# Kernel optimization log

Measured on AMD Instinct MI355X. Metric: run time of the kernel, lower is better.

Reference implementation:

```python
import jax, jax.numpy as jnp
import numpy as np

N_NODES = 10000
N_EDGES = 320000
HIDDEN = 256
HEADS = 8
HEAD_DIM = HIDDEN // HEADS  # 32
NEG_SLOPE = 0.2


def setup_inputs() -> dict:
    key = jax.random.key(0)
    ks = jax.random.split(key, 12)
    x = jax.random.normal(ks[0], (N_NODES, HIDDEN), dtype=jnp.float32)
    edges_idx = jax.random.randint(ks[1], (2, N_EDGES), 0, N_NODES, dtype=jnp.int64)
    s = 1.0 / np.sqrt(HIDDEN)
    # layer 1 params
    W1 = jax.random.normal(ks[2], (HIDDEN, HEADS * HEAD_DIM), dtype=jnp.float32) * s
    a_src1 = jax.random.normal(ks[3], (HEADS, HEAD_DIM), dtype=jnp.float32) * s
    a_dst1 = jax.random.normal(ks[4], (HEADS, HEAD_DIM), dtype=jnp.float32) * s
    b1 = jnp.zeros((HEADS * HEAD_DIM,), dtype=jnp.float32)
    # layer 2 params
    W2 = jax.random.normal(ks[5], (HIDDEN, HEADS * HEAD_DIM), dtype=jnp.float32) * s
    a_src2 = jax.random.normal(ks[6], (HEADS, HEAD_DIM), dtype=jnp.float32) * s
    a_dst2 = jax.random.normal(ks[7], (HEADS, HEAD_DIM), dtype=jnp.float32) * s
    b2 = jnp.zeros((HEADS * HEAD_DIM,), dtype=jnp.float32)
    return {"x": x, "edges_idx": edges_idx,
            "W1": W1, "a_src1": a_src1, "a_dst1": a_dst1, "b1": b1,
            "W2": W2, "a_src2": a_src2, "a_dst2": a_dst2, "b2": b2}


def gat_conv(x, src, dst, W, a_src, a_dst, b):
    """PyG GATConv (concat=True, negative_slope=0.2), dropout in eval mode."""
    N = x.shape[0]
    h = (x @ W).reshape(N, HEADS, HEAD_DIM)          # [N,H,C]
    alpha_s = jnp.einsum('nhc,hc->nh', h, a_src)     # [N,H]
    alpha_d = jnp.einsum('nhc,hc->nh', h, a_dst)     # [N,H]
    e = alpha_s[src] + alpha_d[dst]                  # [E,H]
    e = jnp.where(e > 0, e, NEG_SLOPE * e)           # leaky_relu
    # scatter-softmax over incoming edges of each dst node
    m = jax.ops.segment_max(e, dst, num_segments=N)  # [N,H]
    ex = jnp.exp(e - m[dst])                         # [E,H]
    denom = jax.ops.segment_sum(ex, dst, num_segments=N)  # [N,H]
    alpha = ex / (denom[dst] + 1e-16)                # [E,H]
    msg = h[src] * alpha[:, :, None]                 # [E,H,C]
    out = jax.ops.segment_sum(msg, dst, num_segments=N)   # [N,H,C]
    return out.reshape(N, HEADS * HEAD_DIM) + b


def reference(x, edges_idx, W1, a_src1, a_dst1, b1, W2, a_src2, a_dst2, b2):
    src = edges_idx[0]
    dst = edges_idx[1]
    h = gat_conv(x, src, dst, W1, a_src1, a_dst1, b1)
    h = jax.nn.elu(h)
    out = gat_conv(h, src, dst, W2, a_src2, a_dst2, b2)
    return out
```

## Files before the change

kernel.cpp:

```cpp
#include <hip/hip_runtime.h>
#include <hip/hip_bf16.h>
#include <hip/hip_fp16.h>

#define N_NODES 10000
#define N_EDGES 320000
#define HIDDEN 256
#define HEADS 8
#define HEAD_DIM 32
#define NEG_SLOPE 0.2f
#define CAP 80

typedef __attribute__((ext_vector_type(8))) short short8;
typedef __attribute__((ext_vector_type(8))) _Float16 half8;
typedef __attribute__((ext_vector_type(4))) float f32x4;

__device__ __forceinline__ void bf16_split(float v, unsigned short& hi, unsigned short& lo) {
    __hip_bfloat16 hb = __float2bfloat16(v);
    float hf = __bfloat162float(hb);
    __hip_bfloat16 lb = __float2bfloat16(v - hf);
    hi = *reinterpret_cast<unsigned short*>(&hb);
    lo = *reinterpret_cast<unsigned short*>(&lb);
}

__global__ __launch_bounds__(256) void prep_kernel(
    const float* __restrict__ W1, const float* __restrict__ W2,
    const int* __restrict__ src, const int* __restrict__ dst,
    unsigned short* __restrict__ w1h, unsigned short* __restrict__ w1l,
    unsigned short* __restrict__ w2h, unsigned short* __restrict__ w2l,
    int* __restrict__ counts, int* __restrict__ csr_src) {
    int b = blockIdx.x;
    int tid = threadIdx.x;
    if (b < 512) {
        int i = b * 256 + tid;
        int which = i >> 16;
        int rem = i & 0xFFFF;
        int k = rem >> 8, n = rem & 255;
        const float* W = which ? W2 : W1;
        unsigned short* wh = which ? w2h : w1h;
        unsigned short* wl = which ? w2l : w1l;
        unsigned short h, l;
        bf16_split(W[k * 256 + n], h, l);
        wh[n * 256 + k] = h;
        wl[n * 256 + k] = l;
    } else {
        int e = (b - 512) * 256 + tid;
        int d = dst[e];
        int rank = atomicAdd(&counts[d], 1);
        csr_src[d * CAP + rank] = src[e];
    }
}

template <int AFP32>
__global__ __launch_bounds__(256) void gemm_mfma_kernel(
    const float* __restrict__ Axf,
    const unsigned short* __restrict__ Ah, const unsigned short* __restrict__ Al,
    const unsigned short* __restrict__ BhT, const unsigned short* __restrict__ BlT,
    _Float16* __restrict__ hH, const float* __restrict__ a_src,
    const float* __restrict__ a_dst, float* __restrict__ alpha_s,
    float* __restrict__ alpha_d) {
    __shared__ __align__(16) unsigned short sAh[80 * 40];
    __shared__ __align__(16) unsigned short sAl[80 * 40];
    __shared__ __align__(16) unsigned short sBh[128 * 40];
    __shared__ __align__(16) unsigned short sBl[128 * 40];
    __shared__ __align__(16) _Float16 sOut[80 * 264];
    const int tid = threadIdx.x;
    const int w = tid >> 6, lane = tid & 63;
    const int col = lane & 15, quad = lane >> 4;
    const int m0 = blockIdx.y * 80, n0 = blockIdx.x * 128;

    f32x4 acc[5][2] = {};

    float4 raf[2][3];
    uint4 rau[2][3];
    uint4 rb[2][4];

#define LOAD_A(k0, SS)                                                          \
    if (AFP32) {                                                                \
        _Pragma("unroll") for (int i = 0; i < 3; ++i) {                         \
            int t = tid + i * 256;                                              \
            if (t < 640) {                                                      \
                int row = t >> 3, seg = t & 7;                                  \
                raf[SS][i] = *(const float4*)&Axf[(size_t)(m0 + row) * 256 + (k0) + seg * 4]; \
            }                                                                   \
        }                                                                       \
    } else {                                                                    \
        _Pragma("unroll") for (int i = 0; i < 3; ++i) {                         \
            int t = tid + i * 256;                                              \
            if (t < 640) {                                                      \
                int tt = t < 320 ? t : t - 320;                                 \
                int row = tt >> 2, seg = tt & 3;                                \
                const unsigned short* P = t < 320 ? Ah : Al;                    \
                rau[SS][i] = *(const uint4*)&P[(size_t)(m0 + row) * 256 + (k0) + seg * 8]; \
            }                                                                   \
        }                                                                       \
    }
#define LOAD_B(k0, SS)                                                          \
    _Pragma("unroll") for (int i = 0; i < 4; ++i) {                             \
        int t = tid + i * 256;                                                  \
        int tt = t < 512 ? t : t - 512;                                         \
        int row = tt >> 2, seg = tt & 3;                                        \
        const unsigned short* P = t < 512 ? BhT : BlT;                          \
        rb[SS][i] = *(const uint4*)&P[(size_t)(n0 + row) * 256 + (k0) + seg * 8]; \
    }
#define WRITE_A(SS)                                                             \
    if (AFP32) {                                                                \
        _Pragma("unroll") for (int i = 0; i < 3; ++i) {                         \
            int t = tid + i * 256;                                              \
            if (t < 640) {                                                      \
                int row = t >> 3, seg = t & 7;                                  \
                float4 v = raf[SS][i];                                          \
                ushort4 hh, ll;                                                 \
                unsigned short hb, lb;                                          \
                bf16_split(v.x, hb, lb); hh.x = hb; ll.x = lb;                  \
                bf16_split(v.y, hb, lb); hh.y = hb; ll.y = lb;                  \
                bf16_split(v.z, hb, lb); hh.z = hb; ll.z = lb;                  \
                bf16_split(v.w, hb, lb); hh.w = hb; ll.w = lb;                  \
                *(ushort4*)&sAh[row * 40 + seg * 4] = hh;                       \
                *(ushort4*)&sAl[row * 40 + seg * 4] = ll;                       \
            }                                                                   \
        }                                                                       \
    } else {                                                                    \
        _Pragma("unroll") for (int i = 0; i < 3; ++i) {                         \
            int t = tid + i * 256;                                              \
            if (t < 640) {                                                      \
                int tt = t < 320 ? t : t - 320;                                 \
                int row = tt >> 2, seg = tt & 3;                                \
                unsigned short* Sp = t < 320 ? sAh : sAl;                       \
                *(uint4*)&Sp[row * 40 + seg * 8] = rau[SS][i];                  \
            }                                                                   \
        }                                                                       \
    }
#define WRITE_B(SS)                                                             \
    _Pragma("unroll") for (int i = 0; i < 4; ++i) {                             \
        int t = tid + i * 256;                                                  \
        int tt = t < 512 ? t : t - 512;                                         \
        int row = tt >> 2, seg = tt & 3;                                        \
        unsigned short* Sp = t < 512 ? sBh : sBl;                               \
        *(uint4*)&Sp[row * 40 + seg * 8] = rb[SS][i];                           \
    }

    LOAD_A(0, 0)
    LOAD_B(0, 0)
    LOAD_A(32, 1)
    LOAD_B(32, 1)

#pragma unroll
    for (int ks = 0; ks < 8; ++ks) {
        WRITE_A(ks & 1)
        WRITE_B(ks & 1)
        __syncthreads();

        if (ks < 6) {
            LOAD_A((ks + 2) * 32, ks & 1)
            LOAD_B((ks + 2) * 32, ks & 1)
        }

        short8 bh0 = *(const short8*)&sBh[(w * 32 + col) * 40 + quad * 8];
        short8 bl0 = *(const short8*)&sBl[(w * 32 + col) * 40 + quad * 8];
        short8 bh1 = *(const short8*)&sBh[(w * 32 + 16 + col) * 40 + quad * 8];
        short8 bl1 = *(const short8*)&sBl[(w * 32 + 16 + col) * 40 + quad * 8];
#pragma unroll
        for (int rt = 0; rt < 5; ++rt) {
            short8 ah = *(const short8*)&sAh[(rt * 16 + col) * 40 + quad * 8];
            short8 al = *(const short8*)&sAl[(rt * 16 + col) * 40 + quad * 8];
            acc[rt][0] = __builtin_amdgcn_mfma_f32_16x16x32_bf16(ah, bh0, acc[rt][0], 0, 0, 0);
            acc[rt][0] = __builtin_amdgcn_mfma_f32_16x16x32_bf16(ah, bl0, acc[rt][0], 0, 0, 0);
            acc[rt][0] = __builtin_amdgcn_mfma_f32_16x16x32_bf16(al, bh0, acc[rt][0], 0, 0, 0);
            acc[rt][1] = __builtin_amdgcn_mfma_f32_16x16x32_bf16(ah, bh1, acc[rt][1], 0, 0, 0);
            acc[rt][1] = __builtin_amdgcn_mfma_f32_16x16x32_bf16(ah, bl1, acc[rt][1], 0, 0, 0);
            acc[rt][1] = __builtin_amdgcn_mfma_f32_16x16x32_bf16(al, bh1, acc[rt][1], 0, 0, 0);
        }
        __syncthreads();
    }
#undef LOAD_A
#undef LOAD_B
#undef WRITE_A
#undef WRITE_B

    const int head = blockIdx.x * 4 + w;
    float as0 = a_src[n0 + w * 32 + col];
    float as1 = a_src[n0 + w * 32 + 16 + col];
    float ad0 = a_dst[n0 + w * 32 + col];
    float ad1 = a_dst[n0 + w * 32 + 16 + col];
#pragma unroll
    for (int rt = 0; rt < 5; ++rt) {
#pragma unroll
        for (int r = 0; r < 4; ++r) {
            int row = rt * 16 + quad * 4 + r;
            sOut[row * 264 + w * 32 + col]      = (_Float16)acc[rt][0][r];
            sOut[row * 264 + w * 32 + 16 + col] = (_Float16)acc[rt][1][r];
            float ps = acc[rt][0][r] * as0 + acc[rt][1][r] * as1;
            float pd = acc[rt][0][r] * ad0 + acc[rt][1][r] * ad1;
#pragma unroll
            for (int m = 1; m < 16; m <<= 1) {
                ps += __shfl_xor(ps, m);
                pd += __shfl_xor(pd, m);
            }
            if (col == 0) {
                int gm = m0 + row;
                alpha_s[gm * HEADS + head] = ps;
                alpha_d[gm * HEADS + head] = pd;
            }
        }
    }
    __syncthreads();
#pragma unroll
    for (int i = 0; i < 5; ++i) {
        int t = tid + i * 256;
        int row = t >> 4, seg = t & 15;
        *(half8*)&hH[(size_t)(m0 + row) * 256 + n0 + seg * 8] =
            *(const half8*)&sOut[row * 264 + seg * 8];
    }
}

__global__ __launch_bounds__(256) void aggregate_kernel(
    const int* __restrict__ counts, const int* __restrict__ csr_src,
    const float* __restrict__ alpha_s, const float* __restrict__ alpha_d,
    const _Float16* __restrict__ hH, const float* __restrict__ bias,
    float* __restrict__ outf, unsigned short* __restrict__ oh,
    unsigned short* __restrict__ ol, int mode) {
    const int tid = threadIdx.x;
    const int w = tid >> 6, lane = tid & 63;
    const int ph = blockIdx.x / 2500;
    const int d = (blockIdx.x - ph * 2500) * 4 + w;
    const int q = lane >> 4, fl = lane & 15;
    const int hd = ph * 4 + (fl >> 2);
    const float ad = alpha_d[d * HEADS + hd];
    const int n = counts[d];
    const int* __restrict__ bucket = csr_src + d * CAP;
    const int qb = q * 4;

    const _Float16* hp = hH + ph * 128 + fl * 8;
    float acc[8] = {};
    float den = 0.f;

    int4 s0_ = make_int4(0, 0, 0, 0), s1_ = s0_, s2_ = s0_, s3_ = s0_, s4_ = s0_;
    if (n > 0)  s0_ = *(const int4*)&bucket[qb];
    if (n > 16) s1_ = *(const int4*)&bucket[qb + 16];
    if (n > 32) s2_ = *(const int4*)&bucket[qb + 32];
    if (n > 48) s3_ = *(const int4*)&bucket[qb + 48];
    if (n > 64) s4_ = *(const int4*)&bucket[qb + 64];

#define AGG_DECL(t) float al##t##0, al##t##1, al##t##2, al##t##3;               \
                    half8 hv##t##0, hv##t##1, hv##t##2, hv##t##3;
    AGG_DECL(0) AGG_DECL(1) AGG_DECL(2) AGG_DECL(3) AGG_DECL(4)

#define AGG_CLAMP(x) ((x) < 0 ? 0 : ((x) > 9999 ? 9999 : (x)))
#define AGG_GATHER(t, sv)                                                       \
    {                                                                           \
        int i0_ = AGG_CLAMP((sv).x), i1_ = AGG_CLAMP((sv).y);                   \
        int i2_ = AGG_CLAMP((sv).z), i3_ = AGG_CLAMP((sv).w);                   \
        al##t##0 = alpha_s[i0_ * HEADS + hd];                                   \
        al##t##1 = alpha_s[i1_ * HEADS + hd];                                   \
        al##t##2 = alpha_s[i2_ * HEADS + hd];                                   \
        al##t##3 = alpha_s[i3_ * HEADS + hd];                                   \
        hv##t##0 = *(const half8*)&hp[(size_t)i0_ * HIDDEN];                    \
        hv##t##1 = *(const half8*)&hp[(size_t)i1_ * HIDDEN];                    \
        hv##t##2 = *(const half8*)&hp[(size_t)i2_ * HIDDEN];                    \
        hv##t##3 = *(const half8*)&hp[(size_t)i3_ * HIDDEN];                    \
    }
#define AGG_COMPUTE(t, base)                                                    \
    {                                                                           \
        int b0_ = (base) + qb;                                                  \
        float e0 = al##t##0 + ad; e0 = e0 > 0.f ? e0 : NEG_SLOPE * e0;          \
        float e1 = al##t##1 + ad; e1 = e1 > 0.f ? e1 : NEG_SLOPE * e1;          \
        float e2 = al##t##2 + ad; e2 = e2 > 0.f ? e2 : NEG_SLOPE * e2;          \
        float e3 = al##t##3 + ad; e3 = e3 > 0.f ? e3 : NEG_SLOPE * e3;          \
        if (b0_ >= n)     e0 = -1e30f;                                          \
        if (b0_ + 1 >= n) e1 = -1e30f;                                          \
        if (b0_ + 2 >= n) e2 = -1e30f;                                          \
        if (b0_ + 3 >= n) e3 = -1e30f;                                          \
        float ev0 = __expf(e0), ev1 = __expf(e1);                               \
        float ev2 = __expf(e2), ev3 = __expf(e3);                               \
        den += (ev0 + ev1) + (ev2 + ev3);                                       \
        _Pragma("unroll") for (int j = 0; j < 8; ++j)                           \
            acc[j] += (float)hv##t##0[j] * ev0 + (float)hv##t##1[j] * ev1 +     \
                      (float)hv##t##2[j] * ev2 + (float)hv##t##3[j] * ev3;      \
    }

    if (n > 0)  AGG_GATHER(0, s0_)
    if (n > 16) AGG_GATHER(1, s1_)
    if (n > 0)  AGG_COMPUTE(0, 0)
    if (n > 32) AGG_GATHER(2, s2_)
    if (n > 16) AGG_COMPUTE(1, 16)
    if (n > 48) AGG_GATHER(3, s3_)
    if (n > 32) AGG_COMPUTE(2, 32)
    if (n > 64) AGG_GATHER(4, s4_)
    if (n > 48) AGG_COMPUTE(3, 48)
    if (n > 64) AGG_COMPUTE(4, 64)

#undef AGG_DECL
#undef AGG_CLAMP
#undef AGG_GATHER
#undef AGG_COMPUTE

#pragma unroll
    for (int j = 0; j < 8; ++j) acc[j] += __shfl_xor(acc[j], 16);
    den += __shfl_xor(den, 16);
#pragma unroll
    for (int j = 0; j < 8; ++j) acc[j] += __shfl_xor(acc[j], 32);
    den += __shfl_xor(den, 32);

    if (q == 0) {
        float inv = 1.f / (den + 1e-16f);
        float v[8];
#pragma unroll
        for (int j = 0; j < 8; ++j)
            v[j] = acc[j] * inv + bias[ph * 128 + fl * 8 + j];
        size_t oidx = (size_t)d * HIDDEN + ph * 128 + fl * 8;
        if (mode == 1) {
            unsigned short hb[8], lb[8];
#pragma unroll
            for (int j = 0; j < 8; ++j) {
                v[j] = v[j] > 0.f ? v[j] : (__expf(v[j]) - 1.f);
                bf16_split(v[j], hb[j], lb[j]);
            }
            *(ushort4*)&oh[oidx]     = make_ushort4(hb[0], hb[1], hb[2], hb[3]);
            *(ushort4*)&oh[oidx + 4] = make_ushort4(hb[4], hb[5], hb[6], hb[7]);
            *(ushort4*)&ol[oidx]     = make_ushort4(lb[0], lb[1], lb[2], lb[3]);
            *(ushort4*)&ol[oidx + 4] = make_ushort4(lb[4], lb[5], lb[6], lb[7]);
        } else {
            *(float4*)&outf[oidx]     = make_float4(v[0], v[1], v[2], v[3]);
            *(float4*)&outf[oidx + 4] = make_float4(v[4], v[5], v[6], v[7]);
        }
    }
}

extern "C" void kernel_launch(void* const* d_in, const int* in_sizes, int n_in,
                              void* d_out, int out_size, void* d_ws, size_t ws_size,
                              hipStream_t stream) {
    const float* x      = (const float*)d_in[0];
    const int*   edges  = (const int*)d_in[1];
    const float* W1     = (const float*)d_in[2];
    const float* as1    = (const float*)d_in[3];
    const float* ad1    = (const float*)d_in[4];
    const float* b1     = (const float*)d_in[5];
    const float* W2     = (const float*)d_in[6];
    const float* as2    = (const float*)d_in[7];
    const float* ad2    = (const float*)d_in[8];
    const float* b2     = (const float*)d_in[9];
    float* out = (float*)d_out;

    const int* src = edges;
    const int* dst = edges + N_EDGES;

    const size_t NF = (size_t)N_NODES * HIDDEN;
    const size_t NH = (size_t)N_NODES * HEADS;

    char* base = (char*)d_ws;
    _Float16* hH = (_Float16*)base;             base += NF * 2;
    unsigned short* x2h = (unsigned short*)base; base += NF * 2;
    unsigned short* x2l = (unsigned short*)base; base += NF * 2;
    float* alpha_s = (float*)base;              base += NH * 4;
    float* alpha_d = (float*)base;              base += NH * 4;
    unsigned short* w1h = (unsigned short*)base; base += 65536 * 2;
    unsigned short* w1l = (unsigned short*)base; base += 65536 * 2;
    unsigned short* w2h = (unsigned short*)base; base += 65536 * 2;
    unsigned short* w2l = (unsigned short*)base; base += 65536 * 2;
    int* csr_src = (int*)base;                  base += (size_t)N_NODES * CAP * 4;
    int* counts  = (int*)base;                  base += (size_t)N_NODES * 4;

    dim3 gemm_grid(2, 125);
    const int EB = (N_EDGES + 255) / 256;
    const int AGG_B = 2500 * 2;

    hipMemsetAsync(counts, 0, N_NODES * sizeof(int), stream);
    prep_kernel<<<512 + EB, 256, 0, stream>>>(W1, W2, src, dst,
                                              w1h, w1l, w2h, w2l, counts, csr_src);

    gemm_mfma_kernel<1><<<gemm_grid, 256, 0, stream>>>(
        x, nullptr, nullptr, w1h, w1l, hH, as1, ad1, alpha_s, alpha_d);
    aggregate_kernel<<<AGG_B, 256, 0, stream>>>(counts, csr_src, alpha_s, alpha_d,
                                                hH, b1, nullptr, x2h, x2l, 1);

    gemm_mfma_kernel<0><<<gemm_grid, 256, 0, stream>>>(
        nullptr, x2h, x2l, w2h, w2l, hH, as2, ad2, alpha_s, alpha_d);
    aggregate_kernel<<<AGG_B, 256, 0, stream>>>(counts, csr_src, alpha_s, alpha_d,
                                                hH, b2, out, nullptr, nullptr, 0);
}
```

Baseline: 198.3 us.

## Fuse prep, GEMM and aggregation into two persistent kernels with grid barriers

Replaces the memset-plus-five-launch sequence with two persistent kernels of 250 blocks × 512 threads. Inside them, software grid barriers (atomic counter plus spin) separate the prep, GEMM and aggregation phases. The intent is to remove kernel launch gaps and tail effects between stages. Only 4 of 8 waves do MFMA work in the GEMM phase, and aggregation runs as a grid-stride loop over fewer resident waves. That lowers the latency hiding available for the gather-heavy aggregation. The barrier also relies on all 250 blocks being co-resident.

```diff
diff --git a/kernel.cpp b/kernel.cpp
--- a/kernel.cpp
+++ b/kernel.cpp
@@ -9,6 +9,8 @@
 #define HEAD_DIM 32
 #define NEG_SLOPE 0.2f
 #define CAP 80
+#define NBLK 250
+#define TPB 512
 
 typedef __attribute__((ext_vector_type(8))) short short8;
 typedef __attribute__((ext_vector_type(8))) _Float16 half8;
@@ -22,16 +24,27 @@
     lo = *reinterpret_cast<unsigned short*>(&lb);
 }
 
-__global__ __launch_bounds__(256) void prep_kernel(
+__device__ __forceinline__ void grid_barrier(int* ctr) {
+    __syncthreads();
+    if (threadIdx.x == 0) {
+        __threadfence();
+        atomicAdd(ctr, 1);
+        while (__hip_atomic_load(ctr, __ATOMIC_RELAXED, __HIP_MEMORY_SCOPE_AGENT) < NBLK) {
+            __builtin_amdgcn_s_sleep(2);
+        }
+        __threadfence();
+    }
+    __syncthreads();
+}
+
+__device__ __forceinline__ void prep_phase(
+    int b, int tid,
     const float* __restrict__ W1, const float* __restrict__ W2,
     const int* __restrict__ src, const int* __restrict__ dst,
     unsigned short* __restrict__ w1h, unsigned short* __restrict__ w1l,
     unsigned short* __restrict__ w2h, unsigned short* __restrict__ w2l,
     int* __restrict__ counts, int* __restrict__ csr_src) {
-    int b = blockIdx.x;
-    int tid = threadIdx.x;
-    if (b < 512) {
-        int i = b * 256 + tid;
+    for (int i = b * TPB + tid; i < 131072; i += NBLK * TPB) {
         int which = i >> 16;
         int rem = i & 0xFFFF;
         int k = rem >> 8, n = rem & 255;
@@ -42,8 +55,8 @@
         bf16_split(W[k * 256 + n], h, l);
         wh[n * 256 + k] = h;
         wl[n * 256 + k] = l;
-    } else {
-        int e = (b - 512) * 256 + tid;
+    }
+    for (int e = b * TPB + tid; e < N_EDGES; e += NBLK * TPB) {
         int d = dst[e];
         int rank = atomicAdd(&counts[d], 1);
         csr_src[d * CAP + rank] = src[e];
@@ -51,7 +64,8 @@
 }
 
 template <int AFP32>
-__global__ __launch_bounds__(256) void gemm_mfma_kernel(
+__device__ __forceinline__ void gemm_phase(
+    int b, int tid,
     const float* __restrict__ Axf,
     const unsigned short* __restrict__ Ah, const unsigned short* __restrict__ Al,
     const unsigned short* __restrict__ BhT, const unsigned short* __restrict__ BlT,
@@ -63,29 +77,28 @@
     __shared__ __align__(16) unsigned short sBh[128 * 40];
     __shared__ __align__(16) unsigned short sBl[128 * 40];
     __shared__ __align__(16) _Float16 sOut[80 * 264];
-    const int tid = threadIdx.x;
+
     const int w = tid >> 6, lane = tid & 63;
     const int col = lane & 15, quad = lane >> 4;
-    const int m0 = blockIdx.y * 80, n0 = blockIdx.x * 128;
+    const int m0 = (b >> 1) * 80, n0 = (b & 1) * 128;
 
     f32x4 acc[5][2] = {};
-
-    float4 raf[2][3];
-    uint4 rau[2][3];
-    uint4 rb[2][4];
+    float4 raf[2][2];
+    uint4 rau[2][2];
+    uint4 rb[2][2];
 
 #define LOAD_A(k0, SS)                                                          \
     if (AFP32) {                                                                \
-        _Pragma("unroll") for (int i = 0; i < 3; ++i) {                         \
-            int t = tid + i * 256;                                              \
+        _Pragma("unroll") for (int i = 0; i < 2; ++i) {                         \
+            int t = tid + i * 512;                                              \
             if (t < 640) {                                                      \
                 int row = t >> 3, seg = t & 7;                                  \
                 raf[SS][i] = *(const float4*)&Axf[(size_t)(m0 + row) * 256 + (k0) + seg * 4]; \
             }                                                                   \
         }                                                                       \
     } else {                                                                    \
-        _Pragma("unroll") for (int i = 0; i < 3; ++i) {                         \
-            int t = tid + i * 256;                                              \
+        _Pragma("unroll") for (int i = 0; i < 2; ++i) {                         \
+            int t = tid + i * 512;                                              \
             if (t < 640) {                                                      \
                 int tt = t < 320 ? t : t - 320;                                 \
                 int row = tt >> 2, seg = tt & 3;                                \
@@ -95,8 +108,8 @@
         }                                                                       \
     }
 #define LOAD_B(k0, SS)                                                          \
-    _Pragma("unroll") for (int i = 0; i < 4; ++i) {                             \
-        int t = tid + i * 256;                                                  \
+    _Pragma("unroll") for (int i = 0; i < 2; ++i) {                             \
+        int t = tid + i * 512;                                                  \
         int tt = t < 512 ? t : t - 512;                                         \
         int row = tt >> 2, seg = tt & 3;                                        \
         const unsigned short* P = t < 512 ? BhT : BlT;                          \
@@ -104,8 +117,8 @@
     }
 #define WRITE_A(SS)                                                             \
     if (AFP32) {                                                                \
-        _Pragma("unroll") for (int i = 0; i < 3; ++i) {                         \
-            int t = tid + i * 256;                                              \
+        _Pragma("unroll") for (int i = 0; i < 2; ++i) {                         \
+            int t = tid + i * 512;                                              \
             if (t < 640) {                                                      \
                 int row = t >> 3, seg = t & 7;                                  \
                 float4 v = raf[SS][i];                                          \
@@ -120,8 +133,8 @@
             }                                                                   \
         }                                                                       \
     } else {                                                                    \
-        _Pragma("unroll") for (int i = 0; i < 3; ++i) {                         \
-            int t = tid + i * 256;                                              \
+        _Pragma("unroll") for (int i = 0; i < 2; ++i) {                         \
+            int t = tid + i * 512;                                              \
             if (t < 640) {                                                      \
                 int tt = t < 320 ? t : t - 320;                                 \
                 int row = tt >> 2, seg = tt & 3;                                \
@@ -131,8 +144,8 @@
         }                                                                       \
     }
 #define WRITE_B(SS)                                                             \
-    _Pragma("unroll") for (int i = 0; i < 4; ++i) {                             \
-        int t = tid + i * 256;                                                  \
+    _Pragma("unroll") for (int i = 0; i < 2; ++i) {                             \
+        int t = tid + i * 512;                                                  \
         int tt = t < 512 ? t : t - 512;                                         \
         int row = tt >> 2, seg = tt & 3;                                        \
         unsigned short* Sp = t < 512 ? sBh : sBl;                               \
@@ -155,20 +168,22 @@
             LOAD_B((ks + 2) * 32, ks & 1)
         }
 
-        short8 bh0 = *(const short8*)&sBh[(w * 32 + col) * 40 + quad * 8];
-        short8 bl0 = *(const short8*)&sBl[(w * 32 + col) * 40 + quad * 8];
-        short8 bh1 = *(const short8*)&sBh[(w * 32 + 16 + col) * 40 + quad * 8];
-        short8 bl1 = *(const short8*)&sBl[(w * 32 + 16 + col) * 40 + quad * 8];
-#pragma unroll
-        for (int rt = 0; rt < 5; ++rt) {
-            short8 ah = *(const short8*)&sAh[(rt * 16 + col) * 40 + quad * 8];
-            short8 al = *(const short8*)&sAl[(rt * 16 + col) * 40 + quad * 8];
-            acc[rt][0] = __builtin_amdgcn_mfma_f32_16x16x32_bf16(ah, bh0, acc[rt][0], 0, 0, 0);
-            acc[rt][0] = __builtin_amdgcn_mfma_f32_16x16x32_bf16(ah, bl0, acc[rt][0], 0, 0, 0);
-            acc[rt][0] = __builtin_amdgcn_mfma_f32_16x16x32_bf16(al, bh0, acc[rt][0], 0, 0, 0);
-            acc[rt][1] = __builtin_amdgcn_mfma_f32_16x16x32_bf16(ah, bh1, acc[rt][1], 0, 0, 0);
-            acc[rt][1] = __builtin_amdgcn_mfma_f32_16x16x32_bf16(ah, bl1, acc[rt][1], 0, 0, 0);
-            acc[rt][1] = __builtin_amdgcn_mfma_f32_16x16x32_bf16(al, bh1, acc[rt][1], 0, 0, 0);
+        if (w < 4) {
+            short8 bh0 = *(const short8*)&sBh[(w * 32 + col) * 40 + quad * 8];
+            short8 bl0 = *(const short8*)&sBl[(w * 32 + col) * 40 + quad * 8];
+            short8 bh1 = *(const short8*)&sBh[(w * 32 + 16 + col) * 40 + quad * 8];
+            short8 bl1 = *(const short8*)&sBl[(w * 32 + 16 + col) * 40 + quad * 8];
+#pragma unroll
+            for (int rt = 0; rt < 5; ++rt) {
+                short8 ah = *(const short8*)&sAh[(rt * 16 + col) * 40 + quad * 8];
+                short8 al = *(const short8*)&sAl[(rt * 16 + col) * 40 + quad * 8];
+                acc[rt][0] = __builtin_amdgcn_mfma_f32_16x16x32_bf16(ah, bh0, acc[rt][0], 0, 0, 0);
+                acc[rt][0] = __builtin_amdgcn_mfma_f32_16x16x32_bf16(ah, bl0, acc[rt][0], 0, 0, 0);
+                acc[rt][0] = __builtin_amdgcn_mfma_f32_16x16x32_bf16(al, bh0, acc[rt][0], 0, 0, 0);
+                acc[rt][1] = __builtin_amdgcn_mfma_f32_16x16x32_bf16(ah, bh1, acc[rt][1], 0, 0, 0);
+                acc[rt][1] = __builtin_amdgcn_mfma_f32_16x16x32_bf16(ah, bl1, acc[rt][1], 0, 0, 0);
+                acc[rt][1] = __builtin_amdgcn_mfma_f32_16x16x32_bf16(al, bh1, acc[rt][1], 0, 0, 0);
+            }
         }
         __syncthreads();
     }
@@ -177,95 +192,77 @@
 #undef WRITE_A
 #undef WRITE_B
 
-    const int head = blockIdx.x * 4 + w;
-    float as0 = a_src[n0 + w * 32 + col];
-    float as1 = a_src[n0 + w * 32 + 16 + col];
-    float ad0 = a_dst[n0 + w * 32 + col];
-    float ad1 = a_dst[n0 + w * 32 + 16 + col];
-#pragma unroll
-    for (int rt = 0; rt < 5; ++rt) {
-#pragma unroll
-        for (int r = 0; r < 4; ++r) {
-            int row = rt * 16 + quad * 4 + r;
-            sOut[row * 264 + w * 32 + col]      = (_Float16)acc[rt][0][r];
-            sOut[row * 264 + w * 32 + 16 + col] = (_Float16)acc[rt][1][r];
-            float ps = acc[rt][0][r] * as0 + acc[rt][1][r] * as1;
-            float pd = acc[rt][0][r] * ad0 + acc[rt][1][r] * ad1;
-#pragma unroll
-            for (int m = 1; m < 16; m <<= 1) {
-                ps += __shfl_xor(ps, m);
-                pd += __shfl_xor(pd, m);
+    if (w < 4) {
+        const int head = (b & 1) * 4 + w;
+        float as0 = a_src[n0 + w * 32 + col];
+        float as1 = a_src[n0 + w * 32 + 16 + col];
+        float ad0 = a_dst[n0 + w * 32 + col];
+        float ad1 = a_dst[n0 + w * 32 + 16 + col];
+#pragma unroll
+        for (int rt = 0; rt < 5; ++rt) {
+#pragma unroll
+            for (int r = 0; r < 4; ++r) {
+                int row = rt * 16 + quad * 4 + r;
+                sOut[row * 264 + w * 32 + col]      = (_Float16)acc[rt][0][r];
+                sOut[row * 264 + w * 32 + 16 + col] = (_Float16)acc[rt][1][r];
+                float ps = acc[rt][0][r] * as0 + acc[rt][1][r] * as1;
+                float pd = acc[rt][0][r] * ad0 + acc[rt][1][r] * ad1;
+#pragma unroll
+                for (int m = 1; m < 16; m <<= 1) {
+                    ps += __shfl_xor(ps, m);
+                    pd += __shfl_xor(pd, m);
+                }
+                if (col == 0) {
+                    int gm = m0 + row;
+                    alpha_s[gm * HEADS + head] = ps;
+                    alpha_d[gm * HEADS + head] = pd;
+                }
             }
-            if (col == 0) {
-                int gm = m0 + row;
-                alpha_s[gm * HEADS + head] = ps;
-                alpha_d[gm * HEADS + head] = pd;
-            }
         }
     }
     __syncthreads();
 #pragma unroll
-    for (int i = 0; i < 5; ++i) {
-        int t = tid + i * 256;
-        int row = t >> 4, seg = t & 15;
-        *(half8*)&hH[(size_t)(m0 + row) * 256 + n0 + seg * 8] =
-            *(const half8*)&sOut[row * 264 + seg * 8];
-    }
-}
-
-__global__ __launch_bounds__(256) void aggregate_kernel(
+    for (int i = 0; i < 3; ++i) {
+        int t = tid + i * 512;
+        if (t < 1280) {
+            int row = t >> 4, seg = t & 15;
+            *(half8*)&hH[(size_t)(m0 + row) * 256 + n0 + seg * 8] =
+                *(const half8*)&sOut[row * 264 + seg * 8];
+        }
+    }
+}
+
+template <int MODE>
+__device__ __forceinline__ void agg_phase(
+    int b, int tid,
     const int* __restrict__ counts, const int* __restrict__ csr_src,
     const float* __restrict__ alpha_s, const float* __restrict__ alpha_d,
     const _Float16* __restrict__ hH, const float* __restrict__ bias,
     float* __restrict__ outf, unsigned short* __restrict__ oh,
-    unsigned short* __restrict__ ol, int mode) {
-    const int tid = threadIdx.x;
+    unsigned short* __restrict__ ol) {
     const int w = tid >> 6, lane = tid & 63;
-    const int ph = blockIdx.x / 2500;
-    const int d = (blockIdx.x - ph * 2500) * 4 + w;
     const int q = lane >> 4, fl = lane & 15;
-    const int hd = ph * 4 + (fl >> 2);
-    const float ad = alpha_d[d * HEADS + hd];
-    const int n = counts[d];
-    const int* __restrict__ bucket = csr_src + d * CAP;
     const int qb = q * 4;
-
-    const _Float16* hp = hH + ph * 128 + fl * 8;
-    float acc[8] = {};
-    float den = 0.f;
-
-    int4 s0_ = make_int4(0, 0, 0, 0), s1_ = s0_, s2_ = s0_, s3_ = s0_, s4_ = s0_;
-    if (n > 0)  s0_ = *(const int4*)&bucket[qb];
-    if (n > 16) s1_ = *(const int4*)&bucket[qb + 16];
-    if (n > 32) s2_ = *(const int4*)&bucket[qb + 32];
-    if (n > 48) s3_ = *(const int4*)&bucket[qb + 48];
-    if (n > 64) s4_ = *(const int4*)&bucket[qb + 64];
-
-#define AGG_DECL(t) float al##t##0, al##t##1, al##t##2, al##t##3;               \
-                    half8 hv##t##0, hv##t##1, hv##t##2, hv##t##3;
-    AGG_DECL(0) AGG_DECL(1) AGG_DECL(2) AGG_DECL(3) AGG_DECL(4)
+    const int wg = b * 8 + w;
 
 #define AGG_CLAMP(x) ((x) < 0 ? 0 : ((x) > 9999 ? 9999 : (x)))
-#define AGG_GATHER(t, sv)                                                       \
+#define AGG_ROUND(sv, base)                                                     \
     {                                                                           \
         int i0_ = AGG_CLAMP((sv).x), i1_ = AGG_CLAMP((sv).y);                   \
         int i2_ = AGG_CLAMP((sv).z), i3_ = AGG_CLAMP((sv).w);                   \
-        al##t##0 = alpha_s[i0_ * HEADS + hd];                                   \
-        al##t##1 = alpha_s[i1_ * HEADS + hd];                                   \
-        al##t##2 = alpha_s[i2_ * HEADS + hd];                                   \
-        al##t##3 = alpha_s[i3_ * HEADS + hd];                                   \
-        hv##t##0 = *(const half8*)&hp[(size_t)i0_ * HIDDEN];                    \
-        hv##t##1 = *(const half8*)&hp[(size_t)i1_ * HIDDEN];                    \
-        hv##t##2 = *(const half8*)&hp[(size_t)i2_ * HIDDEN];                    \
-        hv##t##3 = *(const half8*)&hp[(size_t)i3_ * HIDDEN];                    \
-    }
-#define AGG_COMPUTE(t, base)                                                    \
-    {                                                                           \
+        float al0 = alpha_s[i0_ * HEADS + hd];                                  \
+        float al1 = alpha_s[i1_ * HEADS + hd];                                  \
+        float al2 = alpha_s[i2_ * HEADS + hd];                                  \
+        float al3 = alpha_s[i3_ * HEADS + hd];                                  \
+        half8 h0 = *(const half8*)&hp[(size_t)i0_ * HIDDEN];                    \
+        half8 h1 = *(const half8*)&hp[(size_t)i1_ * HIDDEN];                    \
+        half8 h2 = *(const half8*)&hp[(size_t)i2_ * HIDDEN];                    \
+        half8 h3 = *(const half8*)&hp[(size_t)i3_ * HIDDEN];                    \
         int b0_ = (base) + qb;                                                  \
-        float e0 = al##t##0 + ad; e0 = e0 > 0.f ? e0 : NEG_SLOPE * e0;          \
-        float e1 = al##t##1 + ad; e1 = e1 > 0.f ? e1 : NEG_SLOPE * e1;          \
-        float e2 = al##t##2 + ad; e2 = e2 > 0.f ? e2 : NEG_SLOPE * e2;          \
-        float e3 = al##t##3 + ad; e3 = e3 > 0.f ? e3 : NEG_SLOPE * e3;          \
+        float e0 = al0 + ad; e0 = e0 > 0.f ? e0 : NEG_SLOPE * e0;               \
+        float e1 = al1 + ad; e1 = e1 > 0.f ? e1 : NEG_SLOPE * e1;               \
+        float e2 = al2 + ad; e2 = e2 > 0.f ? e2 : NEG_SLOPE * e2;               \
+        float e3 = al3 + ad; e3 = e3 > 0.f ? e3 : NEG_SLOPE * e3;               \
         if (b0_ >= n)     e0 = -1e30f;                                          \
         if (b0_ + 1 >= n) e1 = -1e30f;                                          \
         if (b0_ + 2 >= n) e2 = -1e30f;                                          \
@@ -274,56 +271,98 @@
         float ev2 = __expf(e2), ev3 = __expf(e3);                               \
         den += (ev0 + ev1) + (ev2 + ev3);                                       \
         _Pragma("unroll") for (int j = 0; j < 8; ++j)                           \
-            acc[j] += (float)hv##t##0[j] * ev0 + (float)hv##t##1[j] * ev1 +     \
-                      (float)hv##t##2[j] * ev2 + (float)hv##t##3[j] * ev3;      \
-    }
-
-    if (n > 0)  AGG_GATHER(0, s0_)
-    if (n > 16) AGG_GATHER(1, s1_)
-    if (n > 0)  AGG_COMPUTE(0, 0)
-    if (n > 32) AGG_GATHER(2, s2_)
-    if (n > 16) AGG_COMPUTE(1, 16)
-    if (n > 48) AGG_GATHER(3, s3_)
-    if (n > 32) AGG_COMPUTE(2, 32)
-    if (n > 64) AGG_GATHER(4, s4_)
-    if (n > 48) AGG_COMPUTE(3, 48)
-    if (n > 64) AGG_COMPUTE(4, 64)
-
-#undef AGG_DECL
+            acc[j] += (float)h0[j] * ev0 + (float)h1[j] * ev1 +                 \
+                      (float)h2[j] * ev2 + (float)h3[j] * ev3;                  \
+    }
+
+    for (int task = wg; task < 2 * N_NODES; task += NBLK * 8) {
+        const int ph = task >= N_NODES ? 1 : 0;
+        const int d = task - ph * N_NODES;
+        const int hd = ph * 4 + (fl >> 2);
+        const float ad = alpha_d[d * HEADS + hd];
+        const int n = counts[d];
+        const int* __restrict__ bucket = csr_src + d * CAP;
+        const _Float16* hp = hH + ph * 128 + fl * 8;
+        float acc[8] = {};
+        float den = 0.f;
+
+        int4 s0_ = *(const int4*)&bucket[qb];
+        int4 s1_ = *(const int4*)&bucket[qb + 16];
+        int4 s2_ = *(const int4*)&bucket[qb + 32];
+        int4 s3_ = *(const int4*)&bucket[qb + 48];
+
+        AGG_ROUND(s0_, 0)
+        AGG_ROUND(s1_, 16)
+        AGG_ROUND(s2_, 32)
+        AGG_ROUND(s3_, 48)
+        if (n > 64) {
+            int4 s4_ = *(const int4*)&bucket[qb + 64];
+            AGG_ROUND(s4_, 64)
+        }
+
+#pragma unroll
+        for (int j = 0; j < 8; ++j) acc[j] += __shfl_xor(acc[j], 16);
+        den += __shfl_xor(den, 16);
+#pragma unroll
+        for (int j = 0; j < 8; ++j) acc[j] += __shfl_xor(acc[j], 32);
+        den += __shfl_xor(den, 32);
+
+        if (q == 0) {
+            float inv = 1.f / (den + 1e-16f);
+            float v[8];
+#pragma unroll
+            for (int j = 0; j < 8; ++j)
+                v[j] = acc[j] * inv + bias[ph * 128 + fl * 8 + j];
+            size_t oidx = (size_t)d * HIDDEN + ph * 128 + fl * 8;
+            if (MODE == 1) {
+                unsigned short hb[8], lb[8];
+#pragma unroll
+                for (int j = 0; j < 8; ++j) {
+                    v[j] = v[j] > 0.f ? v[j] : (__expf(v[j]) - 1.f);
+                    bf16_split(v[j], hb[j], lb[j]);
+                }
+                *(ushort4*)&oh[oidx]     = make_ushort4(hb[0], hb[1], hb[2], hb[3]);
+                *(ushort4*)&oh[oidx + 4] = make_ushort4(hb[4], hb[5], hb[6], hb[7]);
+                *(ushort4*)&ol[oidx]     = make_ushort4(lb[0], lb[1], lb[2], lb[3]);
+                *(ushort4*)&ol[oidx + 4] = make_ushort4(lb[4], lb[5], lb[6], lb[7]);
+            } else {
+                *(float4*)&outf[oidx]     = make_float4(v[0], v[1], v[2], v[3]);
+                *(float4*)&outf[oidx + 4] = make_float4(v[4], v[5], v[6], v[7]);
+            }
+        }
+    }
 #undef AGG_CLAMP
-#undef AGG_GATHER
-#undef AGG_COMPUTE
-
-#pragma unroll
-    for (int j = 0; j < 8; ++j) acc[j] += __shfl_xor(acc[j], 16);
-    den += __shfl_xor(den, 16);
-#pragma unroll
-    for (int j = 0; j < 8; ++j) acc[j] += __shfl_xor(acc[j], 32);
-    den += __shfl_xor(den, 32);
-
-    if (q == 0) {
-        float inv = 1.f / (den + 1e-16f);
-        float v[8];
-#pragma unroll
-        for (int j = 0; j < 8; ++j)
-            v[j] = acc[j] * inv + bias[ph * 128 + fl * 8 + j];
-        size_t oidx = (size_t)d * HIDDEN + ph * 128 + fl * 8;
-        if (mode == 1) {
-            unsigned short hb[8], lb[8];
-#pragma unroll
-            for (int j = 0; j < 8; ++j) {
-                v[j] = v[j] > 0.f ? v[j] : (__expf(v[j]) - 1.f);
-                bf16_split(v[j], hb[j], lb[j]);
-            }
-            *(ushort4*)&oh[oidx]     = make_ushort4(hb[0], hb[1], hb[2], hb[3]);
-            *(ushort4*)&oh[oidx + 4] = make_ushort4(hb[4], hb[5], hb[6], hb[7]);
-            *(ushort4*)&ol[oidx]     = make_ushort4(lb[0], lb[1], lb[2], lb[3]);
-            *(ushort4*)&ol[oidx + 4] = make_ushort4(lb[4], lb[5], lb[6], lb[7]);
-        } else {
-            *(float4*)&outf[oidx]     = make_float4(v[0], v[1], v[2], v[3]);
-            *(float4*)&outf[oidx + 4] = make_float4(v[4], v[5], v[6], v[7]);
-        }
-    }
+#undef AGG_ROUND
+}
+
+__global__ __launch_bounds__(TPB) void layer1_kernel(
+    const float* x, const int* src, const int* dst,
+    const float* W1, const float* W2,
+    const float* as1, const float* ad1, const float* b1,
+    unsigned short* w1h, unsigned short* w1l,
+    unsigned short* w2h, unsigned short* w2l,
+    int* counts, int* csr_src,
+    _Float16* hH, float* alpha_s, float* alpha_d,
+    unsigned short* x2h, unsigned short* x2l, int* gbar) {
+    const int b = blockIdx.x, tid = threadIdx.x;
+    prep_phase(b, tid, W1, W2, src, dst, w1h, w1l, w2h, w2l, counts, csr_src);
+    grid_barrier(&gbar[0]);
+    gemm_phase<1>(b, tid, x, nullptr, nullptr, w1h, w1l, hH, as1, ad1, alpha_s, alpha_d);
+    grid_barrier(&gbar[1]);
+    agg_phase<1>(b, tid, counts, csr_src, alpha_s, alpha_d, hH, b1, nullptr, x2h, x2l);
+}
+
+__global__ __launch_bounds__(TPB) void layer2_kernel(
+    const unsigned short* x2h, const unsigned short* x2l,
+    const unsigned short* w2h, const unsigned short* w2l,
+    const float* as2, const float* ad2, const float* b2,
+    const int* counts, const int* csr_src,
+    _Float16* hH, float* alpha_s, float* alpha_d,
+    float* out, int* gbar) {
+    const int b = blockIdx.x, tid = threadIdx.x;
+    gemm_phase<0>(b, tid, nullptr, x2h, x2l, w2h, w2l, hH, as2, ad2, alpha_s, alpha_d);
+    grid_barrier(&gbar[2]);
+    agg_phase<0>(b, tid, counts, csr_src, alpha_s, alpha_d, hH, b2, out, nullptr, nullptr);
 }
 
 extern "C" void kernel_launch(void* const* d_in, const int* in_sizes, int n_in,
@@ -359,22 +398,14 @@
     unsigned short* w2l = (unsigned short*)base; base += 65536 * 2;
     int* csr_src = (int*)base;                  base += (size_t)N_NODES * CAP * 4;
     int* counts  = (int*)base;                  base += (size_t)N_NODES * 4;
-
-    dim3 gemm_grid(2, 125);
-    const int EB = (N_EDGES + 255) / 256;
-    const int AGG_B = 2500 * 2;
-
-    hipMemsetAsync(counts, 0, N_NODES * sizeof(int), stream);
-    prep_kernel<<<512 + EB, 256, 0, stream>>>(W1, W2, src, dst,
-                                              w1h, w1l, w2h, w2l, counts, csr_src);
-
-    gemm_mfma_kernel<1><<<gemm_grid, 256, 0, stream>>>(
-        x, nullptr, nullptr, w1h, w1l, hH, as1, ad1, alpha_s, alpha_d);
-    aggregate_kernel<<<AGG_B, 256, 0, stream>>>(counts, csr_src, alpha_s, alpha_d,
-                                                hH, b1, nullptr, x2h, x2l, 1);
-
-    gemm_mfma_kernel<0><<<gemm_grid, 256, 0, stream>>>(
-        nullptr, x2h, x2l, w2h, w2l, hH, as2, ad2, alpha_s, alpha_d);
-    aggregate_kernel<<<AGG_B, 256, 0, stream>>>(counts, csr_src, alpha_s, alpha_d,
-                                                hH, b2, out, nullptr, nullptr, 0);
-}
+    int* gbar    = (int*)base;                  base += 8 * 4;
+
+    hipMemsetAsync(counts, 0, N_NODES * sizeof(int) + 8 * sizeof(int), stream);
+
+    layer1_kernel<<<NBLK, TPB, 0, stream>>>(x, src, dst, W1, W2, as1, ad1, b1,
+                                            w1h, w1l, w2h, w2l, counts, csr_src,
+                                            hH, alpha_s, alpha_d, x2h, x2l, gbar);
+    layer2_kernel<<<NBLK, TPB, 0, stream>>>(x2h, x2l, w2h, w2l, as2, ad2, b2,
+                                            counts, csr_src, hH, alpha_s, alpha_d,
+                                            out, gbar);
+}
```

Result: slower. 296.4 us (+49.5%).

## Use 512-thread GEMM blocks splitting row tiles, alias LDS, hoist CSR loads

Applied to the files above, without the earlier changes.

The MFMA GEMM moves from 4 to 8 waves per block. Each pair of waves shares a 32-column slice, with one wave doing 3 row tiles and the other 2, which cuts per-wave accumulator and staging registers. The A/B staging buffers and the output staging buffer now alias one shared-memory array, shrinking LDS per block so more blocks can be resident. In the aggregation kernel the first four CSR index loads are issued unconditionally before the count is known, and the fifth load moves into its guarded branch, so fetch latency overlaps with the count load. The cost is an uneven 3/2 split across the wave pair and speculative index reads.

```diff
diff --git a/kernel.cpp b/kernel.cpp
--- a/kernel.cpp
+++ b/kernel.cpp
@@ -51,41 +51,44 @@
 }
 
 template <int AFP32>
-__global__ __launch_bounds__(256) void gemm_mfma_kernel(
+__global__ __launch_bounds__(512) void gemm_mfma_kernel(
     const float* __restrict__ Axf,
     const unsigned short* __restrict__ Ah, const unsigned short* __restrict__ Al,
     const unsigned short* __restrict__ BhT, const unsigned short* __restrict__ BlT,
     _Float16* __restrict__ hH, const float* __restrict__ a_src,
     const float* __restrict__ a_dst, float* __restrict__ alpha_s,
     float* __restrict__ alpha_d) {
-    __shared__ __align__(16) unsigned short sAh[80 * 40];
-    __shared__ __align__(16) unsigned short sAl[80 * 40];
-    __shared__ __align__(16) unsigned short sBh[128 * 40];
-    __shared__ __align__(16) unsigned short sBl[128 * 40];
-    __shared__ __align__(16) _Float16 sOut[80 * 264];
+    __shared__ __align__(16) char smem[42240];
+    unsigned short* sAh = (unsigned short*)smem;
+    unsigned short* sAl = (unsigned short*)(smem + 6400);
+    unsigned short* sBh = (unsigned short*)(smem + 12800);
+    unsigned short* sBl = (unsigned short*)(smem + 23040);
+    _Float16* sOut = (_Float16*)smem;
+
     const int tid = threadIdx.x;
     const int w = tid >> 6, lane = tid & 63;
+    const int c = w & 3, g = w >> 2;
+    const int rtbase = g ? 3 : 0, nrt = g ? 2 : 3;
     const int col = lane & 15, quad = lane >> 4;
     const int m0 = blockIdx.y * 80, n0 = blockIdx.x * 128;
 
-    f32x4 acc[5][2] = {};
-
-    float4 raf[2][3];
-    uint4 rau[2][3];
-    uint4 rb[2][4];
+    f32x4 acc[3][2] = {};
+    float4 raf[2][2];
+    uint4 rau[2][2];
+    uint4 rb[2][2];
 
 #define LOAD_A(k0, SS)                                                          \
     if (AFP32) {                                                                \
-        _Pragma("unroll") for (int i = 0; i < 3; ++i) {                         \
-            int t = tid + i * 256;                                              \
+        _Pragma("unroll") for (int i = 0; i < 2; ++i) {                         \
+            int t = tid + i * 512;                                              \
             if (t < 640) {                                                      \
                 int row = t >> 3, seg = t & 7;                                  \
                 raf[SS][i] = *(const float4*)&Axf[(size_t)(m0 + row) * 256 + (k0) + seg * 4]; \
             }                                                                   \
         }                                                                       \
     } else {                                                                    \
-        _Pragma("unroll") for (int i = 0; i < 3; ++i) {                         \
-            int t = tid + i * 256;                                              \
+        _Pragma("unroll") for (int i = 0; i < 2; ++i) {                         \
+            int t = tid + i * 512;                                              \
             if (t < 640) {                                                      \
                 int tt = t < 320 ? t : t - 320;                                 \
                 int row = tt >> 2, seg = tt & 3;                                \
@@ -95,8 +98,8 @@
         }                                                                       \
     }
 #define LOAD_B(k0, SS)                                                          \
-    _Pragma("unroll") for (int i = 0; i < 4; ++i) {                             \
-        int t = tid + i * 256;                                                  \
+    _Pragma("unroll") for (int i = 0; i < 2; ++i) {                             \
+        int t = tid + i * 512;                                                  \
         int tt = t < 512 ? t : t - 512;                                         \
         int row = tt >> 2, seg = tt & 3;                                        \
         const unsigned short* P = t < 512 ? BhT : BlT;                          \
@@ -104,8 +107,8 @@
     }
 #define WRITE_A(SS)                                                             \
     if (AFP32) {                                                                \
-        _Pragma("unroll") for (int i = 0; i < 3; ++i) {                         \
-            int t = tid + i * 256;                                              \
+        _Pragma("unroll") for (int i = 0; i < 2; ++i) {                         \
+            int t = tid + i * 512;                                              \
             if (t < 640) {                                                      \
                 int row = t >> 3, seg = t & 7;                                  \
                 float4 v = raf[SS][i];                                          \
@@ -120,8 +123,8 @@
             }                                                                   \
         }                                                                       \
     } else {                                                                    \
-        _Pragma("unroll") for (int i = 0; i < 3; ++i) {                         \
-            int t = tid + i * 256;                                              \
+        _Pragma("unroll") for (int i = 0; i < 2; ++i) {                         \
+            int t = tid + i * 512;                                              \
             if (t < 640) {                                                      \
                 int tt = t < 320 ? t : t - 320;                                 \
                 int row = tt >> 2, seg = tt & 3;                                \
@@ -131,8 +134,8 @@
         }                                                                       \
     }
 #define WRITE_B(SS)                                                             \
-    _Pragma("unroll") for (int i = 0; i < 4; ++i) {                             \
-        int t = tid + i * 256;                                                  \
+    _Pragma("unroll") for (int i = 0; i < 2; ++i) {                             \
+        int t = tid + i * 512;                                                  \
         int tt = t < 512 ? t : t - 512;                                         \
         int row = tt >> 2, seg = tt & 3;                                        \
         unsigned short* Sp = t < 512 ? sBh : sBl;                               \
@@ -155,20 +158,23 @@
             LOAD_B((ks + 2) * 32, ks & 1)
         }
 
-        short8 bh0 = *(const short8*)&sBh[(w * 32 + col) * 40 + quad * 8];
-        short8 bl0 = *(const short8*)&sBl[(w * 32 + col) * 40 + quad * 8];
-        short8 bh1 = *(const short8*)&sBh[(w * 32 + 16 + col) * 40 + quad * 8];
-        short8 bl1 = *(const short8*)&sBl[(w * 32 + 16 + col) * 40 + quad * 8];
-#pragma unroll
-        for (int rt = 0; rt < 5; ++rt) {
-            short8 ah = *(const short8*)&sAh[(rt * 16 + col) * 40 + quad * 8];
-            short8 al = *(const short8*)&sAl[(rt * 16 + col) * 40 + quad * 8];
-            acc[rt][0] = __builtin_amdgcn_mfma_f32_16x16x32_bf16(ah, bh0, acc[rt][0], 0, 0, 0);
-            acc[rt][0] = __builtin_amdgcn_mfma_f32_16x16x32_bf16(ah, bl0, acc[rt][0], 0, 0, 0);
-            acc[rt][0] = __builtin_amdgcn_mfma_f32_16x16x32_bf16(al, bh0, acc[rt][0], 0, 0, 0);
-            acc[rt][1] = __builtin_amdgcn_mfma_f32_16x16x32_bf16(ah, bh1, acc[rt][1], 0, 0, 0);
-            acc[rt][1] = __builtin_amdgcn_mfma_f32_16x16x32_bf16(ah, bl1, acc[rt][1], 0, 0, 0);
-            acc[rt][1] = __builtin_amdgcn_mfma_f32_16x16x32_bf16(al, bh1, acc[rt][1], 0, 0, 0);
+        short8 bh0 = *(const short8*)&sBh[(c * 32 + col) * 40 + quad * 8];
+        short8 bl0 = *(const short8*)&sBl[(c * 32 + col) * 40 + quad * 8];
+        short8 bh1 = *(const short8*)&sBh[(c * 32 + 16 + col) * 40 + quad * 8];
+        short8 bl1 = *(const short8*)&sBl[(c * 32 + 16 + col) * 40 + quad * 8];
+#pragma unroll
+        for (int rt = 0; rt < 3; ++rt) {
+            if (rt < nrt) {
+                int rg = rtbase + rt;
+                short8 ah = *(const short8*)&sAh[(rg * 16 + col) * 40 + quad * 8];
+                short8 al = *(const short8*)&sAl[(rg * 16 + col) * 40 + quad * 8];
+                acc[rt][0] = __builtin_amdgcn_mfma_f32_16x16x32_bf16(ah, bh0, acc[rt][0], 0, 0, 0);
+                acc[rt][0] = __builtin_amdgcn_mfma_f32_16x16x32_bf16(ah, bl0, acc[rt][0], 0, 0, 0);
+                acc[rt][0] = __builtin_amdgcn_mfma_f32_16x16x32_bf16(al, bh0, acc[rt][0], 0, 0, 0);
+                acc[rt][1] = __builtin_amdgcn_mfma_f32_16x16x32_bf16(ah, bh1, acc[rt][1], 0, 0, 0);
+                acc[rt][1] = __builtin_amdgcn_mfma_f32_16x16x32_bf16(ah, bl1, acc[rt][1], 0, 0, 0);
+                acc[rt][1] = __builtin_amdgcn_mfma_f32_16x16x32_bf16(al, bh1, acc[rt][1], 0, 0, 0);
+            }
         }
         __syncthreads();
     }
@@ -177,39 +183,44 @@
 #undef WRITE_A
 #undef WRITE_B
 
-    const int head = blockIdx.x * 4 + w;
-    float as0 = a_src[n0 + w * 32 + col];
-    float as1 = a_src[n0 + w * 32 + 16 + col];
-    float ad0 = a_dst[n0 + w * 32 + col];
-    float ad1 = a_dst[n0 + w * 32 + 16 + col];
-#pragma unroll
-    for (int rt = 0; rt < 5; ++rt) {
-#pragma unroll
-        for (int r = 0; r < 4; ++r) {
-            int row = rt * 16 + quad * 4 + r;
-            sOut[row * 264 + w * 32 + col]      = (_Float16)acc[rt][0][r];
-            sOut[row * 264 + w * 32 + 16 + col] = (_Float16)acc[rt][1][r];
-            float ps = acc[rt][0][r] * as0 + acc[rt][1][r] * as1;
-            float pd = acc[rt][0][r] * ad0 + acc[rt][1][r] * ad1;
-#pragma unroll
-            for (int m = 1; m < 16; m <<= 1) {
-                ps += __shfl_xor(ps, m);
-                pd += __shfl_xor(pd, m);
+    const int head = blockIdx.x * 4 + c;
+    float as0 = a_src[n0 + c * 32 + col];
+    float as1 = a_src[n0 + c * 32 + 16 + col];
+    float ad0 = a_dst[n0 + c * 32 + col];
+    float ad1 = a_dst[n0 + c * 32 + 16 + col];
+#pragma unroll
+    for (int rt = 0; rt < 3; ++rt) {
+        if (rt < nrt) {
+            int rg = rtbase + rt;
+#pragma unroll
+            for (int r = 0; r < 4; ++r) {
+                int row = rg * 16 + quad * 4 + r;
+                sOut[row * 264 + c * 32 + col]      = (_Float16)acc[rt][0][r];
+                sOut[row * 264 + c * 32 + 16 + col] = (_Float16)acc[rt][1][r];
+                float ps = acc[rt][0][r] * as0 + acc[rt][1][r] * as1;
+                float pd = acc[rt][0][r] * ad0 + acc[rt][1][r] * ad1;
+#pragma unroll
+                for (int m = 1; m < 16; m <<= 1) {
+                    ps += __shfl_xor(ps, m);
+                    pd += __shfl_xor(pd, m);
+                }
+                if (col == 0) {
+                    int gm = m0 + row;
+                    alpha_s[gm * HEADS + head] = ps;
+                    alpha_d[gm * HEADS + head] = pd;
+                }
             }
-            if (col == 0) {
-                int gm = m0 + row;
-                alpha_s[gm * HEADS + head] = ps;
-                alpha_d[gm * HEADS + head] = pd;
-            }
         }
     }
     __syncthreads();
 #pragma unroll
-    for (int i = 0; i < 5; ++i) {
-        int t = tid + i * 256;
-        int row = t >> 4, seg = t & 15;
-        *(half8*)&hH[(size_t)(m0 + row) * 256 + n0 + seg * 8] =
-            *(const half8*)&sOut[row * 264 + seg * 8];
+    for (int i = 0; i < 3; ++i) {
+        int t = tid + i * 512;
+        if (t < 1280) {
+            int row = t >> 4, seg = t & 15;
+            *(half8*)&hH[(size_t)(m0 + row) * 256 + n0 + seg * 8] =
+                *(const half8*)&sOut[row * 264 + seg * 8];
+        }
     }
 }
 
@@ -225,21 +236,19 @@
     const int d = (blockIdx.x - ph * 2500) * 4 + w;
     const int q = lane >> 4, fl = lane & 15;
     const int hd = ph * 4 + (fl >> 2);
+    const int qb = q * 4;
+    const int* __restrict__ bucket = csr_src + d * CAP;
+    const _Float16* hp = hH + ph * 128 + fl * 8;
+
+    const int n = counts[d];
     const float ad = alpha_d[d * HEADS + hd];
-    const int n = counts[d];
-    const int* __restrict__ bucket = csr_src + d * CAP;
-    const int qb = q * 4;
-
-    const _Float16* hp = hH + ph * 128 + fl * 8;
+    int4 s0_ = *(const int4*)&bucket[qb];
+    int4 s1_ = *(const int4*)&bucket[qb + 16];
+    int4 s2_ = *(const int4*)&bucket[qb + 32];
+    int4 s3_ = *(const int4*)&bucket[qb + 48];
+
     float acc[8] = {};
     float den = 0.f;
-
-    int4 s0_ = make_int4(0, 0, 0, 0), s1_ = s0_, s2_ = s0_, s3_ = s0_, s4_ = s0_;
-    if (n > 0)  s0_ = *(const int4*)&bucket[qb];
-    if (n > 16) s1_ = *(const int4*)&bucket[qb + 16];
-    if (n > 32) s2_ = *(const int4*)&bucket[qb + 32];
-    if (n > 48) s3_ = *(const int4*)&bucket[qb + 48];
-    if (n > 64) s4_ = *(const int4*)&bucket[qb + 64];
 
 #define AGG_DECL(t) float al##t##0, al##t##1, al##t##2, al##t##3;               \
                     half8 hv##t##0, hv##t##1, hv##t##2, hv##t##3;
@@ -285,9 +294,12 @@
     if (n > 16) AGG_COMPUTE(1, 16)
     if (n > 48) AGG_GATHER(3, s3_)
     if (n > 32) AGG_COMPUTE(2, 32)
-    if (n > 64) AGG_GATHER(4, s4_)
     if (n > 48) AGG_COMPUTE(3, 48)
-    if (n > 64) AGG_COMPUTE(4, 64)
+    if (n > 64) {
+        int4 s4_ = *(const int4*)&bucket[qb + 64];
+        AGG_GATHER(4, s4_)
+        AGG_COMPUTE(4, 64)
+    }
 
 #undef AGG_DECL
 #undef AGG_CLAMP
@@ -368,12 +380,12 @@
     prep_kernel<<<512 + EB, 256, 0, stream>>>(W1, W2, src, dst,
                                               w1h, w1l, w2h, w2l, counts, csr_src);
 
-    gemm_mfma_kernel<1><<<gemm_grid, 256, 0, stream>>>(
+    gemm_mfma_kernel<1><<<gemm_grid, 512, 0, stream>>>(
         x, nullptr, nullptr, w1h, w1l, hH, as1, ad1, alpha_s, alpha_d);
     aggregate_kernel<<<AGG_B, 256, 0, stream>>>(counts, csr_src, alpha_s, alpha_d,
                                                 hH, b1, nullptr, x2h, x2l, 1);
 
-    gemm_mfma_kernel<0><<<gemm_grid, 256, 0, stream>>>(
+    gemm_mfma_kernel<0><<<gemm_grid, 512, 0, stream>>>(
         nullptr, x2h, x2l, w2h, w2l, hH, as2, ad2, alpha_s, alpha_d);
     aggregate_kernel<<<AGG_B, 256, 0, stream>>>(counts, csr_src, alpha_s, alpha_d,
                                                 hH, b2, out, nullptr, nullptr, 0);
```

Result: faster. 189.1 us (-4.6%).
